# Kernel tuning notes

Hardware: AMD Instinct MI355X
Metric: run time of the kernel (lower is better)

Reference implementation:

```python
import jax, jax.numpy as jnp
import numpy as np

LARGE_NEG = -1000000000.0
D_MODEL = 1024
NUM_HEADS = 16
DEPTH = D_MODEL // NUM_HEADS


def setup_inputs() -> dict:
    key = jax.random.key(0)
    ks = jax.random.split(key, 12)
    B, S, D = 4, 2048, D_MODEL
    scale = 1.0 / np.sqrt(D)
    inp = {
        "v": jax.random.normal(ks[0], (B, S, D), jnp.float32),
        "k": jax.random.normal(ks[1], (B, S, D), jnp.float32),
        "q": jax.random.normal(ks[2], (B, S, D), jnp.float32),
        "mask": jax.random.randint(ks[3], (B, 1, 1, S), 0, 2, jnp.int32),
        "Wq": jax.random.normal(ks[4], (D, D), jnp.float32) * scale,
        "bq": jnp.zeros((D,), jnp.float32),
        "Wk": jax.random.normal(ks[5], (D, D), jnp.float32) * scale,
        "bk": jnp.zeros((D,), jnp.float32),
        "Wv": jax.random.normal(ks[6], (D, D), jnp.float32) * scale,
        "bv": jnp.zeros((D,), jnp.float32),
        "Wo": jax.random.normal(ks[7], (D, D), jnp.float32) * scale,
        "bo": jnp.zeros((D,), jnp.float32),
    }
    return inp


def _split_heads(x):
    # [B, S, D] -> [B, H, S, depth]
    B, S, _ = x.shape
    return x.reshape(B, S, NUM_HEADS, DEPTH).transpose(0, 2, 1, 3)


def reference(v, k, q, mask, Wq, bq, Wk, bk, Wv, bv, Wo, bo):
    B, Sq, D = q.shape
    qh = _split_heads(q @ Wq + bq)  # [B,H,Sq,d]
    kh = _split_heads(k @ Wk + bk)  # [B,H,Sk,d]
    vh = _split_heads(v @ Wv + bv)  # [B,H,Sk,d]
    logits = jnp.einsum('bhqd,bhkd->bhqk', qh, kh) / jnp.sqrt(
        jnp.asarray(DEPTH, jnp.float32))
    logits = logits + mask.astype(jnp.float32) * LARGE_NEG
    attn = jax.nn.softmax(logits, axis=-1)
    ctx = jnp.einsum('bhqk,bhkd->bhqd', attn, vh)
    ctx = ctx.transpose(0, 2, 1, 3).reshape(B, Sq, D)  # concat heads
    return ctx @ Wo + bo
```

## Files before the change

### kernel.cpp

```cpp
#include <hip/hip_runtime.h>


typedef unsigned short ushort_t;
typedef __bf16          b16x8 __attribute__((ext_vector_type(8)));
typedef unsigned short  u16x8 __attribute__((ext_vector_type(8)));
typedef unsigned short  u16x4 __attribute__((ext_vector_type(4)));
typedef unsigned int    u32x4 __attribute__((ext_vector_type(4)));
typedef float           f32x4 __attribute__((ext_vector_type(4)));

#define B_ 4
#define S_ 2048
#define D_ 1024
#define H_ 16
#define DEPTH_ 64
#define LOG2E 1.4426950408889634f

__device__ __forceinline__ unsigned short f2bf(float f) {
  unsigned u = __builtin_bit_cast(unsigned, f);
  u += 0x7FFFu + ((u >> 16) & 1u);
  return (unsigned short)(u >> 16);
}

__device__ __forceinline__ unsigned pack_trunc(float lo, float hi) {
#if __has_builtin(__builtin_amdgcn_perm)
  return __builtin_amdgcn_perm(__builtin_bit_cast(unsigned, hi),
                               __builtin_bit_cast(unsigned, lo), 0x07060302u);
#else
  return (__builtin_bit_cast(unsigned, hi) & 0xFFFF0000u) |
         (__builtin_bit_cast(unsigned, lo) >> 16);
#endif
}

#if __has_builtin(__builtin_amdgcn_exp2f)
#define EXP2F(x) __builtin_amdgcn_exp2f(x)
#else
#define EXP2F(x) exp2f(x)
#endif

#define GLD16(gp, lp) __builtin_amdgcn_global_load_lds( \
    (__attribute__((address_space(1))) void*)(gp),       \
    (__attribute__((address_space(3))) void*)(lp), 16, 0, 0)

#define MFMA_BF16(a, b, c) __builtin_amdgcn_mfma_f32_16x16x32_bf16( \
    __builtin_bit_cast(b16x8, (a)), __builtin_bit_cast(b16x8, (b)), (c), 0, 0, 0)


__global__ void cvt_acts_kernel(const float* __restrict__ q, const float* __restrict__ k,
                                const float* __restrict__ v,
                                ushort_t* __restrict__ qb, ushort_t* __restrict__ kb,
                                ushort_t* __restrict__ vb) {
  const float* src = blockIdx.y == 0 ? q : blockIdx.y == 1 ? k : v;
  ushort_t*    dst = blockIdx.y == 0 ? qb : blockIdx.y == 1 ? kb : vb;
  size_t i = ((size_t)blockIdx.x * 256 + threadIdx.x) * 4;
  float4 f = *(const float4*)(src + i);
  u16x4 o;
  o[0] = f2bf(f.x); o[1] = f2bf(f.y); o[2] = f2bf(f.z); o[3] = f2bf(f.w);
  *(u16x4*)(dst + i) = o;
}

__global__ void cvt_wt_kernel(const float* __restrict__ Wq, const float* __restrict__ Wk,
                              const float* __restrict__ Wv, const float* __restrict__ Wo,
                              ushort_t* __restrict__ Wqt, ushort_t* __restrict__ Wkt,
                              ushort_t* __restrict__ Wvt, ushort_t* __restrict__ Wot) {
  __shared__ float t[32][33];
  const int z = blockIdx.y;
  const float* W = z == 0 ? Wq : z == 1 ? Wk : z == 2 ? Wv : Wo;
  ushort_t*   Wt = z == 0 ? Wqt : z == 1 ? Wkt : z == 2 ? Wvt : Wot;
  const int x = threadIdx.x & 31, y0 = threadIdx.x >> 5;
  const int kt = (blockIdx.x & 31) * 32, nt = (blockIdx.x >> 5) * 32;
#pragma unroll
  for (int r = 0; r < 4; r++) {
    int row = y0 + r * 8;
    t[row][x] = W[(size_t)(kt + row) * D_ + nt + x];
  }
  __syncthreads();
#pragma unroll
  for (int r = 0; r < 4; r++) {
    int row = y0 + r * 8;
    Wt[(size_t)(nt + row) * D_ + kt + x] = f2bf(t[x][row]);
  }
}


__device__ __forceinline__ void gemm_core(const ushort_t* __restrict__ A,
                                          const ushort_t* __restrict__ Bt,
                                          ushort_t* As, ushort_t* Bs,
                                          int tm, int tn, f32x4* acc) {
  const int tid = threadIdx.x;
  const int lane = tid & 63, wid = tid >> 6;
  const int wm = (wid >> 1) * 64, wn = (wid & 1) * 64;
  const int srow = lane >> 3;
  const int scol = ((lane & 7) ^ srow) * 8;
  const ushort_t* gA[4];
  const ushort_t* gB[4];
#pragma unroll
  for (int c = 0; c < 4; c++) {
    const int ch = wid * 4 + c;
    gA[c] = A  + (size_t)(tm + ch * 8 + srow) * D_ + scol;
    gB[c] = Bt + (size_t)(tn + ch * 8 + srow) * D_ + scol;
  }
  const int fr = lane & 15, fq = lane >> 4;
#pragma unroll
  for (int i = 0; i < 16; i++) acc[i] = f32x4{0.f, 0.f, 0.f, 0.f};
  for (int k0 = 0; k0 < D_; k0 += 64) {
    __syncthreads();
#pragma unroll
    for (int c = 0; c < 4; c++) {
      const int ch = wid * 4 + c;
      GLD16(gA[c] + k0, As + ch * 512);
      GLD16(gB[c] + k0, Bs + ch * 512);
    }
    __syncthreads();
#pragma unroll
    for (int kh = 0; kh < 2; kh++) {
      const int coff = (((kh * 4 + fq) ^ (fr & 7))) * 8;
      u16x8 af[4], bf[4];
#pragma unroll
      for (int mi = 0; mi < 4; mi++)
        af[mi] = *(const u16x8*)(As + (wm + mi * 16 + fr) * 64 + coff);
#pragma unroll
      for (int ni = 0; ni < 4; ni++)
        bf[ni] = *(const u16x8*)(Bs + (wn + ni * 16 + fr) * 64 + coff);
#pragma unroll
      for (int mi = 0; mi < 4; mi++)
#pragma unroll
        for (int ni = 0; ni < 4; ni++)
          acc[mi * 4 + ni] = MFMA_BF16(af[mi], bf[ni], acc[mi * 4 + ni]);
    }
  }
}

__device__ __forceinline__ int sigma32(int k5) {
  return ((k5 & 15) >> 2) * 8 + ((k5 >> 4) & 1) * 4 + (k5 & 3);
}

__device__ __forceinline__ void gemm_tile_swizzle(int bx, int& tm, int& tn) {
  const int xcd = bx & 7, j = bx >> 3;
  tn = (j & 7) * 128;
  tm = (((j >> 3) << 3) | xcd) * 128;
}

__global__ __launch_bounds__(256, 3) void qkv_gemm_kernel(
    const ushort_t* __restrict__ qb, const ushort_t* __restrict__ kb, const ushort_t* __restrict__ vb,
    const ushort_t* __restrict__ Wqt, const ushort_t* __restrict__ Wkt, const ushort_t* __restrict__ Wvt,
    const float* __restrict__ bq, const float* __restrict__ bk, const float* __restrict__ bv,
    ushort_t* __restrict__ Qh, ushort_t* __restrict__ Kh, ushort_t* __restrict__ Vht) {
  __shared__ __align__(16) ushort_t smem[128 * 136];
  ushort_t* As = smem;
  ushort_t* Bs = smem + 8192;
  const int z = blockIdx.z;
  const ushort_t* A  = z == 0 ? qb : z == 1 ? kb : vb;
  const ushort_t* Bt = z == 0 ? Wqt : z == 1 ? Wkt : Wvt;
  const float* bias  = z == 0 ? bq : z == 1 ? bk : bv;
  int tm, tn;
  gemm_tile_swizzle(blockIdx.x, tm, tn);
  f32x4 acc[16];
  gemm_core(A, Bt, As, Bs, tm, tn, acc);
  const int lane = threadIdx.x & 63, wid = threadIdx.x >> 6;
  const int wm = (wid >> 1) * 64, wn = (wid & 1) * 64;
  const int fr = lane & 15, rq = (lane >> 4) * 4;
  if (z == 2) {
    __syncthreads();
    ushort_t* trans = smem;
#pragma unroll
    for (int ni = 0; ni < 4; ni++) {
      const int n = wn + ni * 16 + fr;
      const float bb = bias[tn + n];
#pragma unroll
      for (int mi = 0; mi < 4; mi++) {
#pragma unroll
        for (int r = 0; r < 4; r++) {
          const int m = wm + mi * 16 + rq + r;
          const int mp = (m & ~31) + sigma32(m & 31);
          trans[n * 136 + mp] = f2bf(acc[mi * 4 + ni][r] + bb);
        }
      }
    }
    __syncthreads();
    const int n = threadIdx.x >> 1, hf = threadIdx.x & 1;
    const int col = tn + n, hh = col >> 6, dd = col & 63;
    const int bI = tm >> 11, sb = (tm & 2047) + hf * 64;
    ushort_t* dst = Vht + ((size_t)(bI * H_ + hh) * DEPTH_ + dd) * S_ + sb;
    const ushort_t* srcp = trans + n * 136 + hf * 64;
#pragma unroll
    for (int i = 0; i < 8; i++)
      *(u16x8*)(dst + i * 8) = *(const u16x8*)(srcp + i * 8);
  } else {
    ushort_t* outp = (z == 0) ? Qh : Kh;
    const float qscale = (z == 0) ? 0.125f * LOG2E : 1.0f;
#pragma unroll
    for (int ni = 0; ni < 4; ni++) {
      const int col = tn + wn + ni * 16 + fr;
      const float bb = bias[col];
      const int h = col >> 6, dd = col & 63;
#pragma unroll
      for (int mi = 0; mi < 4; mi++) {
#pragma unroll
        for (int r = 0; r < 4; r++) {
          const int m = tm + wm + mi * 16 + rq + r;
          const int b = m >> 11, s = m & 2047;
          outp[((size_t)(b * H_ + h) * S_ + s) * DEPTH_ + dd] =
              f2bf((acc[mi * 4 + ni][r] + bb) * qscale);
        }
      }
    }
  }
}

__global__ __launch_bounds__(256, 3) void out_gemm_kernel(
    const ushort_t* __restrict__ ctx, const ushort_t* __restrict__ Wot,
    const float* __restrict__ bo, float* __restrict__ out) {
  __shared__ __align__(16) ushort_t As[8192], Bs[8192];
  int tm, tn;
  gemm_tile_swizzle(blockIdx.x, tm, tn);
  f32x4 acc[16];
  gemm_core(ctx, Wot, As, Bs, tm, tn, acc);
  const int lane = threadIdx.x & 63, wid = threadIdx.x >> 6;
  const int wm = (wid >> 1) * 64, wn = (wid & 1) * 64;
  const int fr = lane & 15, rq = (lane >> 4) * 4;
#pragma unroll
  for (int ni = 0; ni < 4; ni++) {
    const int col = tn + wn + ni * 16 + fr;
    const float bb = bo[col];
#pragma unroll
    for (int mi = 0; mi < 4; mi++) {
#pragma unroll
      for (int r = 0; r < 4; r++) {
        const int m = tm + wm + mi * 16 + rq + r;
        out[(size_t)m * D_ + col] = acc[mi * 4 + ni][r] + bb;
      }
    }
  }
}


__global__ __launch_bounds__(256, 4) void attn_kernel(
    const ushort_t* __restrict__ Qh, const ushort_t* __restrict__ Kh,
    const ushort_t* __restrict__ Vht, const int* __restrict__ mask,
    ushort_t* __restrict__ ctx) {
  __shared__ __align__(16) ushort_t Ks[128 * 64];
  __shared__ __align__(16) ushort_t Vs[64 * 128];
  __shared__ __align__(16) float Cm[2048];
  const int tid = threadIdx.x, lane = tid & 63, wid = tid >> 6;
  const int id = blockIdx.x;
  const int xcd = id & 7, j = id >> 3;
  const int qt = j & 15;
  const int bh = xcd * 8 + (j >> 4);
  const int b = bh >> 4, h = bh & 15;
  const size_t base = (size_t)bh * (S_ * DEPTH_);
  const int fr = lane & 15, fq = lane >> 4;

  const int* mrow = mask + b * S_;
#pragma unroll
  for (int i = 0; i < 8; i++) {
    const int idx = tid + i * 256;
    Cm[idx] = mrow[idx] ? -1.4427e9f : 0.0f;
  }

  u16x8 qf[2][2];
#pragma unroll
  for (int nq = 0; nq < 2; nq++)
#pragma unroll
    for (int kc = 0; kc < 2; kc++)
      qf[nq][kc] = *(const u16x8*)(Qh + base +
          (size_t)(qt * 128 + wid * 32 + nq * 16 + fr) * DEPTH_ + kc * 32 + fq * 8);

  u16x8 ones_f;
  {
    const unsigned short o = (fr == 0) ? (unsigned short)0x3F80 : (unsigned short)0;
#pragma unroll
    for (int jj = 0; jj < 8; jj++) ones_f[jj] = o;
  }

  f32x4 Oa[4][2];
  f32x4 lacc[2];
#pragma unroll
  for (int di = 0; di < 4; di++)
#pragma unroll
    for (int nq = 0; nq < 2; nq++) Oa[di][nq] = f32x4{0.f, 0.f, 0.f, 0.f};
#pragma unroll
  for (int nq = 0; nq < 2; nq++) lacc[nq] = f32x4{0.f, 0.f, 0.f, 0.f};

  const int krow = lane >> 3;
  const int kcolL = ((lane & 7) ^ (krow & 7)) * 8;
  const int vrowc = lane >> 4;
  const int koff0 = ((0 + fq) ^ (fr & 7)) * 8;
  const int koff1 = ((4 + fq) ^ (fr & 7)) * 8;

  for (int kt = 0; kt < 16; kt++) {
    __syncthreads();
#pragma unroll
    for (int c = 0; c < 4; c++) {
      const int ch = wid * 4 + c;
      GLD16(Kh + base + (size_t)(kt * 128 + ch * 8 + krow) * DEPTH_ + kcolL, Ks + ch * 512);
      const int vrow = ch * 4 + vrowc;
      const int vcolL = ((lane & 15) ^ (vrow & 15)) * 8;
      GLD16(Vht + base + (size_t)vrow * S_ + kt * 128 + vcolL, Vs + ch * 512);
    }
    __syncthreads();

#pragma unroll
    for (int ks = 0; ks < 4; ks++) {
      const int nk0 = ks * 2, nk1 = nk0 + 1;
      const ushort_t* kr0 = Ks + (nk0 * 16 + fr) * 64;
      const ushort_t* kr1 = Ks + (nk1 * 16 + fr) * 64;
      const u16x8 a00 = *(const u16x8*)(kr0 + koff0);
      const u16x8 a01 = *(const u16x8*)(kr0 + koff1);
      const u16x8 a10 = *(const u16x8*)(kr1 + koff0);
      const u16x8 a11 = *(const u16x8*)(kr1 + koff1);
      f32x4 st0[2], st1[2];
#pragma unroll
      for (int nq = 0; nq < 2; nq++) {
        f32x4 t = f32x4{0.f, 0.f, 0.f, 0.f};
        t = MFMA_BF16(a00, qf[nq][0], t);
        t = MFMA_BF16(a01, qf[nq][1], t);
        st0[nq] = t;
        f32x4 u = f32x4{0.f, 0.f, 0.f, 0.f};
        u = MFMA_BF16(a10, qf[nq][0], u);
        u = MFMA_BF16(a11, qf[nq][1], u);
        st1[nq] = u;
      }
      const f32x4 cm0 = *(const f32x4*)(Cm + kt * 128 + nk0 * 16 + fq * 4);
      const f32x4 cm1 = *(const f32x4*)(Cm + kt * 128 + nk1 * 16 + fq * 4);
      u16x8 pb[2];
#pragma unroll
      for (int nq = 0; nq < 2; nq++) {
#pragma unroll
        for (int r = 0; r < 4; r++) {
          st0[nq][r] = EXP2F(st0[nq][r] + cm0[r]);
          st1[nq][r] = EXP2F(st1[nq][r] + cm1[r]);
        }
        u32x4 pk;
        pk[0] = pack_trunc(st0[nq][0], st0[nq][1]);
        pk[1] = pack_trunc(st0[nq][2], st0[nq][3]);
        pk[2] = pack_trunc(st1[nq][0], st1[nq][1]);
        pk[3] = pack_trunc(st1[nq][2], st1[nq][3]);
        pb[nq] = __builtin_bit_cast(u16x8, pk);
      }
      const int voff = ((ks * 4 + fq) ^ fr) * 8;
#pragma unroll
      for (int di = 0; di < 4; di++) {
        const u16x8 vf = *(const u16x8*)(Vs + (di * 16 + fr) * 128 + voff);
#pragma unroll
        for (int nq = 0; nq < 2; nq++)
          Oa[di][nq] = MFMA_BF16(vf, pb[nq], Oa[di][nq]);
      }
#pragma unroll
      for (int nq = 0; nq < 2; nq++)
        lacc[nq] = MFMA_BF16(ones_f, pb[nq], lacc[nq]);
    }
  }

#pragma unroll
  for (int nq = 0; nq < 2; nq++) {
    const int lv = __builtin_amdgcn_ds_bpermute(fr * 4, __builtin_bit_cast(int, lacc[nq][0]));
    const float inv = 1.0f / __builtin_bit_cast(float, lv);
    const int sg = qt * 128 + wid * 32 + nq * 16 + fr;
    ushort_t* crow = ctx + ((size_t)(b * S_ + sg)) * D_ + h * DEPTH_;
#pragma unroll
    for (int di = 0; di < 4; di++) {
      u16x4 o4;
#pragma unroll
      for (int r = 0; r < 4; r++) o4[r] = f2bf(Oa[di][nq][r] * inv);
      *(u16x4*)(crow + di * 16 + fq * 4) = o4;
    }
  }
}


extern "C" void kernel_launch(void* const* d_in, const int* in_sizes, int n_in,
                              void* d_out, int out_size, void* d_ws, size_t ws_size,
                              hipStream_t stream) {
  const float* v  = (const float*)d_in[0];
  const float* k  = (const float*)d_in[1];
  const float* q  = (const float*)d_in[2];
  const int* mask = (const int*)d_in[3];
  const float* Wq = (const float*)d_in[4];
  const float* bq = (const float*)d_in[5];
  const float* Wk = (const float*)d_in[6];
  const float* bk = (const float*)d_in[7];
  const float* Wv = (const float*)d_in[8];
  const float* bv = (const float*)d_in[9];
  const float* Wo = (const float*)d_in[10];
  const float* bo = (const float*)d_in[11];
  float* out = (float*)d_out;

  char* ws = (char*)d_ws;
  ushort_t* qb  = (ushort_t*)(ws);
  ushort_t* kb  = (ushort_t*)(ws + (size_t)(16u << 20));
  ushort_t* vb  = (ushort_t*)(ws + (size_t)(32u << 20));
  ushort_t* Wqt = (ushort_t*)(ws + (size_t)(48u << 20));
  ushort_t* Wkt = (ushort_t*)(ws + (size_t)(50u << 20));
  ushort_t* Wvt = (ushort_t*)(ws + (size_t)(52u << 20));
  ushort_t* Wot = (ushort_t*)(ws + (size_t)(54u << 20));
  ushort_t* Qh  = (ushort_t*)(ws + (size_t)(56u << 20));
  ushort_t* Kh  = (ushort_t*)(ws + (size_t)(72u << 20));
  ushort_t* Vht = (ushort_t*)(ws + (size_t)(88u << 20));
  ushort_t* ctx = qb;

  cvt_acts_kernel<<<dim3(8192, 3), 256, 0, stream>>>(q, k, v, qb, kb, vb);
  cvt_wt_kernel<<<dim3(1024, 4), 256, 0, stream>>>(Wq, Wk, Wv, Wo, Wqt, Wkt, Wvt, Wot);
  qkv_gemm_kernel<<<dim3(512, 1, 3), 256, 0, stream>>>(qb, kb, vb, Wqt, Wkt, Wvt,
                                                       bq, bk, bv, Qh, Kh, Vht);
  attn_kernel<<<dim3(1024), 256, 0, stream>>>(Qh, Kh, Vht, mask, ctx);
  out_gemm_kernel<<<dim3(512), 256, 0, stream>>>(ctx, Wot, bo, out);
}
```

Before: 323.7 us.

## Merge conversion kernels, fold mask into MFMA accumulator, raise GEMM occupancy

Combines the activation and weight fp32-to-bf16 conversion kernels into one launch, with extra y=3 blocks doing the weight transposes and the surplus blocks exiting early. In attention, the per-block LDS mask table is removed. Mask values are now loaded from global memory into registers each key tile and used as the initial MFMA accumulator, which removes the add before exp2. GEMM launch bounds go from 3 to 4 blocks per CU, which can force register spilling in exchange for higher occupancy.

New measurement: 399.4 us. +23.4%, slower.

```diff
diff --git a/kernel.cpp b/kernel.cpp
--- a/kernel.cpp
+++ b/kernel.cpp
@@ -7,6 +7,7 @@
 typedef unsigned short  u16x4 __attribute__((ext_vector_type(4)));
 typedef unsigned int    u32x4 __attribute__((ext_vector_type(4)));
 typedef float           f32x4 __attribute__((ext_vector_type(4)));
+typedef int             i32x4 __attribute__((ext_vector_type(4)));
 
 #define B_ 4
 #define S_ 2048
@@ -14,6 +15,7 @@
 #define H_ 16
 #define DEPTH_ 64
 #define LOG2E 1.4426950408889634f
+#define MASKC (-1.4426950408889634e9f)
 
 __device__ __forceinline__ unsigned short f2bf(float f) {
   unsigned u = __builtin_bit_cast(unsigned, f);
@@ -45,39 +47,43 @@
     __builtin_bit_cast(b16x8, (a)), __builtin_bit_cast(b16x8, (b)), (c), 0, 0, 0)
 
 
-__global__ void cvt_acts_kernel(const float* __restrict__ q, const float* __restrict__ k,
-                                const float* __restrict__ v,
-                                ushort_t* __restrict__ qb, ushort_t* __restrict__ kb,
-                                ushort_t* __restrict__ vb) {
-  const float* src = blockIdx.y == 0 ? q : blockIdx.y == 1 ? k : v;
-  ushort_t*    dst = blockIdx.y == 0 ? qb : blockIdx.y == 1 ? kb : vb;
-  size_t i = ((size_t)blockIdx.x * 256 + threadIdx.x) * 4;
-  float4 f = *(const float4*)(src + i);
-  u16x4 o;
-  o[0] = f2bf(f.x); o[1] = f2bf(f.y); o[2] = f2bf(f.z); o[3] = f2bf(f.w);
-  *(u16x4*)(dst + i) = o;
-}
-
-__global__ void cvt_wt_kernel(const float* __restrict__ Wq, const float* __restrict__ Wk,
-                              const float* __restrict__ Wv, const float* __restrict__ Wo,
-                              ushort_t* __restrict__ Wqt, ushort_t* __restrict__ Wkt,
-                              ushort_t* __restrict__ Wvt, ushort_t* __restrict__ Wot) {
+__global__ void cvt_kernel(const float* __restrict__ q, const float* __restrict__ k,
+                           const float* __restrict__ v,
+                           const float* __restrict__ Wq, const float* __restrict__ Wk,
+                           const float* __restrict__ Wv, const float* __restrict__ Wo,
+                           ushort_t* __restrict__ qb, ushort_t* __restrict__ kb,
+                           ushort_t* __restrict__ vb,
+                           ushort_t* __restrict__ Wqt, ushort_t* __restrict__ Wkt,
+                           ushort_t* __restrict__ Wvt, ushort_t* __restrict__ Wot) {
   __shared__ float t[32][33];
-  const int z = blockIdx.y;
+  const int y = blockIdx.y;
+  if (y < 3) {
+    const float* src = y == 0 ? q : y == 1 ? k : v;
+    ushort_t*    dst = y == 0 ? qb : y == 1 ? kb : vb;
+    size_t i = ((size_t)blockIdx.x * 256 + threadIdx.x) * 4;
+    float4 f = *(const float4*)(src + i);
+    u16x4 o;
+    o[0] = f2bf(f.x); o[1] = f2bf(f.y); o[2] = f2bf(f.z); o[3] = f2bf(f.w);
+    *(u16x4*)(dst + i) = o;
+    return;
+  }
+  const int x = blockIdx.x;
+  if (x >= 4096) return;
+  const int z = x >> 10, tile = x & 1023;
   const float* W = z == 0 ? Wq : z == 1 ? Wk : z == 2 ? Wv : Wo;
   ushort_t*   Wt = z == 0 ? Wqt : z == 1 ? Wkt : z == 2 ? Wvt : Wot;
-  const int x = threadIdx.x & 31, y0 = threadIdx.x >> 5;
-  const int kt = (blockIdx.x & 31) * 32, nt = (blockIdx.x >> 5) * 32;
+  const int xx = threadIdx.x & 31, y0 = threadIdx.x >> 5;
+  const int kt = (tile & 31) * 32, nt = (tile >> 5) * 32;
 #pragma unroll
   for (int r = 0; r < 4; r++) {
     int row = y0 + r * 8;
-    t[row][x] = W[(size_t)(kt + row) * D_ + nt + x];
+    t[row][xx] = W[(size_t)(kt + row) * D_ + nt + xx];
   }
   __syncthreads();
 #pragma unroll
   for (int r = 0; r < 4; r++) {
     int row = y0 + r * 8;
-    Wt[(size_t)(nt + row) * D_ + kt + x] = f2bf(t[x][row]);
+    Wt[(size_t)(nt + row) * D_ + kt + xx] = f2bf(t[xx][row]);
   }
 }
 
@@ -140,7 +146,7 @@
   tm = (((j >> 3) << 3) | xcd) * 128;
 }
 
-__global__ __launch_bounds__(256, 3) void qkv_gemm_kernel(
+__global__ __launch_bounds__(256, 4) void qkv_gemm_kernel(
     const ushort_t* __restrict__ qb, const ushort_t* __restrict__ kb, const ushort_t* __restrict__ vb,
     const ushort_t* __restrict__ Wqt, const ushort_t* __restrict__ Wkt, const ushort_t* __restrict__ Wvt,
     const float* __restrict__ bq, const float* __restrict__ bk, const float* __restrict__ bv,
@@ -207,7 +213,7 @@
   }
 }
 
-__global__ __launch_bounds__(256, 3) void out_gemm_kernel(
+__global__ __launch_bounds__(256, 4) void out_gemm_kernel(
     const ushort_t* __restrict__ ctx, const ushort_t* __restrict__ Wot,
     const float* __restrict__ bo, float* __restrict__ out) {
   __shared__ __align__(16) ushort_t As[8192], Bs[8192];
@@ -240,7 +246,6 @@
     ushort_t* __restrict__ ctx) {
   __shared__ __align__(16) ushort_t Ks[128 * 64];
   __shared__ __align__(16) ushort_t Vs[64 * 128];
-  __shared__ __align__(16) float Cm[2048];
   const int tid = threadIdx.x, lane = tid & 63, wid = tid >> 6;
   const int id = blockIdx.x;
   const int xcd = id & 7, j = id >> 3;
@@ -251,11 +256,6 @@
   const int fr = lane & 15, fq = lane >> 4;
 
   const int* mrow = mask + b * S_;
-#pragma unroll
-  for (int i = 0; i < 8; i++) {
-    const int idx = tid + i * 256;
-    Cm[idx] = mrow[idx] ? -1.4427e9f : 0.0f;
-  }
 
   u16x8 qf[2][2];
 #pragma unroll
@@ -289,6 +289,10 @@
 
   for (int kt = 0; kt < 16; kt++) {
     __syncthreads();
+    i32x4 mk[8];
+#pragma unroll
+    for (int t = 0; t < 8; t++)
+      mk[t] = *(const i32x4*)(mrow + kt * 128 + t * 16 + fq * 4);
 #pragma unroll
     for (int c = 0; c < 4; c++) {
       const int ch = wid * 4 + c;
@@ -298,6 +302,12 @@
       GLD16(Vht + base + (size_t)vrow * S_ + kt * 128 + vcolL, Vs + ch * 512);
     }
     __syncthreads();
+    f32x4 cmv[8];
+#pragma unroll
+    for (int t = 0; t < 8; t++)
+#pragma unroll
+      for (int r = 0; r < 4; r++)
+        cmv[t][r] = mk[t][r] ? MASKC : 0.0f;
 
 #pragma unroll
     for (int ks = 0; ks < 4; ks++) {
@@ -311,24 +321,22 @@
       f32x4 st0[2], st1[2];
 #pragma unroll
       for (int nq = 0; nq < 2; nq++) {
-        f32x4 t = f32x4{0.f, 0.f, 0.f, 0.f};
+        f32x4 t = cmv[nk0];
         t = MFMA_BF16(a00, qf[nq][0], t);
         t = MFMA_BF16(a01, qf[nq][1], t);
         st0[nq] = t;
-        f32x4 u = f32x4{0.f, 0.f, 0.f, 0.f};
+        f32x4 u = cmv[nk1];
         u = MFMA_BF16(a10, qf[nq][0], u);
         u = MFMA_BF16(a11, qf[nq][1], u);
         st1[nq] = u;
       }
-      const f32x4 cm0 = *(const f32x4*)(Cm + kt * 128 + nk0 * 16 + fq * 4);
-      const f32x4 cm1 = *(const f32x4*)(Cm + kt * 128 + nk1 * 16 + fq * 4);
       u16x8 pb[2];
 #pragma unroll
       for (int nq = 0; nq < 2; nq++) {
 #pragma unroll
         for (int r = 0; r < 4; r++) {
-          st0[nq][r] = EXP2F(st0[nq][r] + cm0[r]);
-          st1[nq][r] = EXP2F(st1[nq][r] + cm1[r]);
+          st0[nq][r] = EXP2F(st0[nq][r]);
+          st1[nq][r] = EXP2F(st1[nq][r]);
         }
         u32x4 pk;
         pk[0] = pack_trunc(st0[nq][0], st0[nq][1]);
@@ -398,8 +406,8 @@
   ushort_t* Vht = (ushort_t*)(ws + (size_t)(88u << 20));
   ushort_t* ctx = qb;
 
-  cvt_acts_kernel<<<dim3(8192, 3), 256, 0, stream>>>(q, k, v, qb, kb, vb);
-  cvt_wt_kernel<<<dim3(1024, 4), 256, 0, stream>>>(Wq, Wk, Wv, Wo, Wqt, Wkt, Wvt, Wot);
+  cvt_kernel<<<dim3(8192, 4), 256, 0, stream>>>(q, k, v, Wq, Wk, Wv, Wo,
+                                                qb, kb, vb, Wqt, Wkt, Wvt, Wot);
   qkv_gemm_kernel<<<dim3(512, 1, 3), 256, 0, stream>>>(qb, kb, vb, Wqt, Wkt, Wvt,
                                                        bq, bk, bv, Qh, Kh, Vht);
   attn_kernel<<<dim3(1024), 256, 0, stream>>>(Qh, Kh, Vht, mask, ctx);
```
